# Kernel optimization log

Measured on AMD Instinct MI355X. Metric: run time of the kernel, lower is better.

## Reference

```python
import jax, jax.numpy as jnp
import numpy as np
import math

D_MODEL = 1024
N_HEAD = 16
D_FF = 4096
N_LAYERS = 4
SEQ = 2048
BATCH = 1
LN_EPS = 1e-5


def _pos_encoding(S, D, dtype):
    pos = jnp.arange(S, dtype=dtype)[:, None]                      # [S,1]
    div = jnp.exp(jnp.arange(0, D, 2, dtype=dtype) * (-math.log(10000.0) / D))
    ang = pos * div                                                 # [S,D/2]
    pe = jnp.stack([jnp.sin(ang), jnp.cos(ang)], axis=-1).reshape(S, D)  # interleave sin/cos
    return pe[:, None, :]                                           # [S,1,D]


def _layernorm(x, g, b):
    mu = jnp.mean(x, axis=-1, keepdims=True)
    var = jnp.mean(jnp.square(x - mu), axis=-1, keepdims=True)
    return (x - mu) * jax.lax.rsqrt(var + LN_EPS) * g + b


def setup_inputs() -> dict:
    key = jax.random.key(0)
    ks = jax.random.split(key, 16)
    f32 = jnp.float32
    L, D, F = N_LAYERS, D_MODEL, D_FF
    s = 0.02
    inp = {
        "X": jax.random.normal(ks[0], (SEQ, BATCH, D), dtype=f32),
        "Wqkv": jax.random.normal(ks[1], (L, 3 * D, D), dtype=f32) * s,
        "bqkv": jnp.zeros((L, 3 * D), dtype=f32),
        "Wo": jax.random.normal(ks[2], (L, D, D), dtype=f32) * s,
        "bo": jnp.zeros((L, D), dtype=f32),
        "ln1_g": jnp.ones((L, D), dtype=f32),
        "ln1_b": jnp.zeros((L, D), dtype=f32),
        "W1": jax.random.normal(ks[3], (L, F, D), dtype=f32) * s,
        "b1": jnp.zeros((L, F), dtype=f32),
        "W2": jax.random.normal(ks[4], (L, D, F), dtype=f32) * s,
        "b2": jnp.zeros((L, D), dtype=f32),
        "ln2_g": jnp.ones((L, D), dtype=f32),
        "ln2_b": jnp.zeros((L, D), dtype=f32),
        "Wdec": jax.random.normal(ks[5], (3, D), dtype=f32) * s,
        "bdec": jnp.zeros((3,), dtype=f32),
        "window_size": 128,
        "nhead": 16,
    }
    return inp


def reference(X, Wqkv, bqkv, Wo, bo, ln1_g, ln1_b, W1, b1, W2, b2, ln2_g, ln2_b, Wdec, bdec, window_size, nhead):
    S, B, D = X.shape
    H = nhead
    hd = D // H
    scale = 1.0 / math.sqrt(hd)

    x = X + _pos_encoding(S, D, X.dtype)  # dropout is identity at eval

    # banded additive mask: allowed iff |i-j| < window_size (triu/tril(-inf) construction)
    idx = jnp.arange(S)
    band = jnp.abs(idx[:, None] - idx[None, :]) < window_size
    mask = jnp.where(band, jnp.array(0.0, X.dtype), jnp.array(-jnp.inf, X.dtype))  # [S,S]

    L = Wqkv.shape[0]
    for l in range(L):
        # self-attention (post-norm encoder layer)
        qkv = jnp.einsum('sbd,ed->sbe', x, Wqkv[l]) + bqkv[l]
        q, k, v = jnp.split(qkv, 3, axis=-1)
        q = q.reshape(S, B, H, hd)
        k = k.reshape(S, B, H, hd)
        v = v.reshape(S, B, H, hd)
        scores = jnp.einsum('sbhd,tbhd->bhst', q, k) * scale + mask  # [B,H,S,S]
        attn = jax.nn.softmax(scores, axis=-1)
        o = jnp.einsum('bhst,tbhd->sbhd', attn, v).reshape(S, B, D)
        o = jnp.einsum('sbd,ed->sbe', o, Wo[l]) + bo[l]
        x = _layernorm(x + o, ln1_g[l], ln1_b[l])
        # feed-forward (relu)
        h = jax.nn.relu(jnp.einsum('sbd,fd->sbf', x, W1[l]) + b1[l])
        ff = jnp.einsum('sbf,df->sbd', h, W2[l]) + b2[l]
        x = _layernorm(x + ff, ln2_g[l], ln2_b[l])

    logits = jnp.einsum('sbd,cd->sbc', x, Wdec) + bdec  # [S,B,3]
    return jax.nn.log_softmax(logits, axis=-1)
```

## Files before the change

kernel.cpp:

```cpp
#include <hip/hip_runtime.h>
#include <hip/hip_bf16.h>
#include <cmath>

typedef __hip_bfloat16 bf16;
typedef __bf16 bf16x8 __attribute__((ext_vector_type(8)));
typedef __bf16 bf16x4 __attribute__((ext_vector_type(4)));
typedef float f32x4 __attribute__((ext_vector_type(4)));

typedef __attribute__((address_space(1))) void void_g;
typedef __attribute__((address_space(3))) void void_l;

#define SEQ 2048
#define DMODEL 1024
#define NHEAD 16
#define HDIM 64
#define DFF 4096
#define WINDOW 128
#define LN_EPS 1e-5f

__device__ __forceinline__ void gl_lds16(const bf16* g, bf16* l) {
    __builtin_amdgcn_global_load_lds((void_g*)(g), (void_l*)(l), 16, 0, 0);
}

__device__ __forceinline__ bf16x8 cvt8(float4 a, float4 b) {
    bf16x8 w;
    w[0] = (__bf16)a.x; w[1] = (__bf16)a.y; w[2] = (__bf16)a.z; w[3] = (__bf16)a.w;
    w[4] = (__bf16)b.x; w[5] = (__bf16)b.y; w[6] = (__bf16)b.z; w[7] = (__bf16)b.w;
    return w;
}

__global__ __launch_bounds__(256)
void add_pe(const float* __restrict__ X, bf16* __restrict__ x) {
    int idx = blockIdx.x * 256 + threadIdx.x;
    int s = idx >> 10, d = idx & 1023;
    float i2 = (float)(d & ~1);
    float div = expf(i2 * (-9.210340371976184f / 1024.0f));
    float ang = (float)s * div;
    float pe = (d & 1) ? cosf(ang) : sinf(ang);
    x[idx] = (bf16)(X[idx] + pe);
}

__global__ __launch_bounds__(256)
void cvt_w_layer(const float* __restrict__ wqkv, const float* __restrict__ wo,
                 const float* __restrict__ w1, const float* __restrict__ w2,
                 bf16* __restrict__ dst)
{
    int i = blockIdx.x * 256 + threadIdx.x;
    const float* src; size_t so;
    if (i < 393216)       { src = wqkv; so = (size_t)i * 8; }
    else if (i < 524288)  { src = wo;   so = (size_t)(i - 393216) * 8; }
    else if (i < 1048576) { src = w1;   so = (size_t)(i - 524288) * 8; }
    else                  { src = w2;   so = (size_t)(i - 1048576) * 8; }
    float4 a = *(const float4*)(src + so);
    float4 b = *(const float4*)(src + so + 4);
    *(bf16x8*)(dst + (size_t)i * 8) = cvt8(a, b);
}


#define G_PROLOGUE(Adecl, Wdecl)                                                 \
    __shared__ __align__(16) bf16 AS[2][128 * 64];                               \
    __shared__ __align__(16) bf16 BS[2][128 * 64];                               \
    const int tid  = threadIdx.x;                                                \
    const int lane = tid & 63;                                                   \
    const int wave = tid >> 6;                                                   \
    const int wm = wave >> 1, wn = wave & 1;                                     \
    const int r = lane & 15, quad = lane >> 4;                                   \
    const int rc = (quad ^ (r & 3)) * 8;                                         \
    f32x4 acc[4][4];                                                             \
    _Pragma("unroll")                                                            \
    for (int i = 0; i < 4; ++i)                                                  \
        _Pragma("unroll")                                                        \
        for (int j = 0; j < 4; ++j) acc[i][j] = (f32x4){0.f, 0.f, 0.f, 0.f};     \
    const bf16* Ap[4]; const bf16* Bp[4];                                        \
    _Pragma("unroll")                                                            \
    for (int i = 0; i < 4; ++i) {                                                \
        int c = tid + 256 * i;                                                   \
        int ks = c >> 9, row = (c >> 2) & 127, kch = (c & 3) ^ (row & 3);        \
        Ap[i] = (Adecl) + (size_t)(m0 + row) * K + ks * 32 + kch * 8;            \
        Bp[i] = (Wdecl) + (size_t)(n0 + row) * K + ks * 32 + kch * 8;            \
    }

#define G_STAGE(koff, Ad, Bd)                                                    \
    _Pragma("unroll")                                                            \
    for (int i = 0; i < 4; ++i)                                                  \
        gl_lds16(Ap[i] + (koff), (Ad) + (size_t)(tid + 256 * i) * 8);            \
    _Pragma("unroll")                                                            \
    for (int i = 0; i < 4; ++i)                                                  \
        gl_lds16(Bp[i] + (koff), (Bd) + (size_t)(tid + 256 * i) * 8);

#define G_KLOOP(Klim)                                                            \
    const int nit = (Klim) / 64;                                                 \
    bf16 *A_c = &AS[0][0], *A_n = &AS[1][0];                                     \
    bf16 *B_c = &BS[0][0], *B_n = &BS[1][0];                                     \
    G_STAGE(0, A_c, B_c)                                                         \
    asm volatile("s_waitcnt vmcnt(0)" ::: "memory");                             \
    __builtin_amdgcn_s_barrier();                                                \
    for (int t = 0; t < nit; ++t) {                                              \
        if (t + 1 < nit) { G_STAGE((t + 1) * 64, A_n, B_n) }                     \
        bf16x8 av[4][2], bv[4][2];                                               \
        _Pragma("unroll")                                                        \
        for (int mf = 0; mf < 4; ++mf)                                           \
            _Pragma("unroll")                                                    \
            for (int kk = 0; kk < 2; ++kk)                                       \
                av[mf][kk] = *(const bf16x8*)(A_c + kk * 4096 +                  \
                              (wm * 64 + mf * 16 + r) * 32 + rc);                \
        _Pragma("unroll")                                                        \
        for (int nf = 0; nf < 4; ++nf)                                           \
            _Pragma("unroll")                                                    \
            for (int kk = 0; kk < 2; ++kk)                                       \
                bv[nf][kk] = *(const bf16x8*)(B_c + kk * 4096 +                  \
                              (wn * 64 + nf * 16 + r) * 32 + rc);                \
        __builtin_amdgcn_s_setprio(1);                                           \
        _Pragma("unroll")                                                        \
        for (int mf = 0; mf < 4; ++mf)                                           \
            _Pragma("unroll")                                                    \
            for (int nf = 0; nf < 4; ++nf)                                       \
                _Pragma("unroll")                                                \
                for (int kk = 0; kk < 2; ++kk)                                   \
                    acc[mf][nf] = __builtin_amdgcn_mfma_f32_16x16x32_bf16(       \
                        av[mf][kk], bv[nf][kk], acc[mf][nf], 0, 0, 0);           \
        __builtin_amdgcn_s_setprio(0);                                           \
        asm volatile("s_waitcnt vmcnt(0)" ::: "memory");                         \
        __builtin_amdgcn_s_barrier();                                            \
        bf16* tA = A_c; A_c = A_n; A_n = tA;                                     \
        bf16* tB = B_c; B_c = B_n; B_n = tB;                                     \
    }

template<int ACT, int SX, int SY, int VOUT>
__global__ __launch_bounds__(256)
void gemm8_bt(const bf16* __restrict__ A, const bf16* __restrict__ W,
              const float* __restrict__ bias, bf16* __restrict__ C,
              bf16* __restrict__ Vt, int M, int N, int K)
{
    const int gx = gridDim.x;
    const int l = blockIdx.y * gx + blockIdx.x;
    const int k = l & 7, j = l >> 3;
    const int xg = gx / SX;
    const int tx = (k % xg) * SX + (j % SX);
    const int ty = (k / xg) * SY + (j / SX);
    const int m0 = ty * 128, n0 = tx * 128;
    G_PROLOGUE(A, W)
    G_KLOOP(K)
    if (VOUT && n0 >= 2048) {
#pragma unroll
        for (int nt = 0; nt < 4; ++nt) {
            int n = n0 + wn * 64 + nt * 16 + r;
            float bv = bias[n];
            int dv = n - 2048;
#pragma unroll
            for (int mt = 0; mt < 4; ++mt) {
                int m = m0 + wm * 64 + mt * 16 + quad * 4;
                bf16x4 pk;
#pragma unroll
                for (int e = 0; e < 4; ++e) pk[e] = (__bf16)(acc[mt][nt][e] + bv);
                *(bf16x4*)(Vt + (size_t)dv * SEQ + m) = pk;
            }
        }
    } else {
#pragma unroll
        for (int nt = 0; nt < 4; ++nt) {
            int n = n0 + wn * 64 + nt * 16 + r;
            float bv = bias[n];
#pragma unroll
            for (int mt = 0; mt < 4; ++mt) {
#pragma unroll
                for (int e = 0; e < 4; ++e) {
                    int m = m0 + wm * 64 + mt * 16 + quad * 4 + e;
                    float v = acc[mt][nt][e] + bv;
                    if (ACT == 1) v = fmaxf(v, 0.f);
                    C[(size_t)m * N + n] = (bf16)v;
                }
            }
        }
    }
}

template<int SPLIT, int SY>
__global__ __launch_bounds__(256)
void gemm8_splitk(const bf16* __restrict__ A, const bf16* __restrict__ Wfull,
                  float* __restrict__ Cacc, int M, int N, int K)
{
    const int gx = gridDim.x, gy = gridDim.y;
    const int l = (blockIdx.z * gy + blockIdx.y) * gx + blockIdx.x;
    const int k = l & 7, j = l >> 3;
    const int yg = gy / SY;
    const int tx = j % gx;
    const int ty = (k % yg) * SY + (j / gx);
    const int tz = k / yg;
    const int m0 = ty * 128, n0 = tx * 128;
    const int Kc = K / SPLIT;
    const bf16* Ab = A + (size_t)tz * Kc;
    const bf16* W = Wfull + (size_t)tz * Kc;
    float* Cz = Cacc + (size_t)tz * M * N;
    G_PROLOGUE(Ab, W)
    G_KLOOP(Kc)
#pragma unroll
    for (int nt = 0; nt < 4; ++nt) {
        int n = n0 + wn * 64 + nt * 16 + r;
#pragma unroll
        for (int mt = 0; mt < 4; ++mt) {
#pragma unroll
            for (int e = 0; e < 4; ++e) {
                int m = m0 + wm * 64 + mt * 16 + quad * 4 + e;
                Cz[(size_t)m * N + n] = acc[mt][nt][e];
            }
        }
    }
}

__global__ __launch_bounds__(256)
void attn_mfma(const bf16* __restrict__ qkv, const bf16* __restrict__ Vt,
               bf16* __restrict__ o)
{
    __shared__ __align__(16) __bf16 Plds[4][16 * 40];
    const int tid = threadIdx.x, lane = tid & 63, w = tid >> 6;
    const int h = blockIdx.x & 15;
    const int qw = (blockIdx.x >> 4) * 64 + w * 16;
    const int r = lane & 15, quad = lane >> 4;
    __bf16* P = Plds[w];

    bf16x8 qa[2];
    {
        const bf16* qrow = qkv + (size_t)(qw + r) * 3072 + h * 64 + quad * 8;
#pragma unroll
        for (int c = 0; c < 2; ++c) {
            bf16x8 t = *(const bf16x8*)(qrow + c * 32);
#pragma unroll
            for (int j = 0; j < 8; ++j) qa[c][j] = (__bf16)((float)t[j] * 0.125f);
        }
    }

    bf16x8 ones;
#pragma unroll
    for (int j = 0; j < 8; ++j) ones[j] = (__bf16)1.0f;

    f32x4 acc[4];
#pragma unroll
    for (int d = 0; d < 4; ++d) acc[d] = (f32x4){0.f, 0.f, 0.f, 0.f};
    float m_run[4], l_run[4];
#pragma unroll
    for (int e = 0; e < 4; ++e) { m_run[e] = -1e30f; l_run[e] = 0.f; }

    int jmin = qw - (WINDOW - 1); if (jmin < 0) jmin = 0;
    int jmax = qw + 15 + (WINDOW - 1); if (jmax > SEQ - 1) jmax = SEQ - 1;

    for (int kt = jmin & ~31; kt <= jmax; kt += 32) {
        f32x4 S[2];
#pragma unroll
        for (int c = 0; c < 2; ++c) {
            const bf16* krow = qkv + (size_t)(kt + 16 * c + r) * 3072 + 1024 + h * 64 + quad * 8;
            bf16x8 kb0 = *(const bf16x8*)(krow);
            bf16x8 kb1 = *(const bf16x8*)(krow + 32);
            f32x4 s = (f32x4){0.f, 0.f, 0.f, 0.f};
            s = __builtin_amdgcn_mfma_f32_16x16x32_bf16(qa[0], kb0, s, 0, 0, 0);
            s = __builtin_amdgcn_mfma_f32_16x16x32_bf16(qa[1], kb1, s, 0, 0, 0);
            S[c] = s;
        }
#pragma unroll
        for (int c = 0; c < 2; ++c)
#pragma unroll
            for (int e = 0; e < 4; ++e) {
                int j = kt + 16 * c + r;
                int i = qw + quad * 4 + e;
                bool valid = (unsigned)(j - i + (WINDOW - 1)) <= (unsigned)(2 * WINDOW - 2);
                S[c][e] = valid ? S[c][e] : -1e30f;
            }
        float alpha[4], mnew[4];
#pragma unroll
        for (int e = 0; e < 4; ++e) {
            float v = fmaxf(S[0][e], S[1][e]);
#pragma unroll
            for (int off = 1; off <= 8; off <<= 1) v = fmaxf(v, __shfl_xor(v, off, 64));
            mnew[e] = fmaxf(m_run[e], v);
            alpha[e] = __expf(m_run[e] - mnew[e]);
            m_run[e] = mnew[e];
        }
#pragma unroll
        for (int c = 0; c < 2; ++c)
#pragma unroll
            for (int e = 0; e < 4; ++e) {
                float p = __expf(S[c][e] - mnew[e]);
                p = (S[c][e] <= -1e29f) ? 0.f : p;
                P[(quad * 4 + e) * 40 + 16 * c + r] = (__bf16)p;
            }
        bf16x8 pa = *(const bf16x8*)(P + r * 40 + quad * 8);
#pragma unroll
        for (int d = 0; d < 4; ++d)
#pragma unroll
            for (int e = 0; e < 4; ++e) acc[d][e] *= alpha[e];
        f32x4 ls = (f32x4){0.f, 0.f, 0.f, 0.f};
        ls = __builtin_amdgcn_mfma_f32_16x16x32_bf16(pa, ones, ls, 0, 0, 0);
#pragma unroll
        for (int e = 0; e < 4; ++e) l_run[e] = l_run[e] * alpha[e] + ls[e];
#pragma unroll
        for (int d = 0; d < 4; ++d) {
            const bf16* vrow = Vt + (size_t)(h * 64 + 16 * d + r) * SEQ + kt + quad * 8;
            bf16x8 vb = *(const bf16x8*)(vrow);
            acc[d] = __builtin_amdgcn_mfma_f32_16x16x32_bf16(pa, vb, acc[d], 0, 0, 0);
        }
    }

#pragma unroll
    for (int d = 0; d < 4; ++d)
#pragma unroll
        for (int e = 0; e < 4; ++e) {
            int i = qw + quad * 4 + e;
            o[(size_t)i * DMODEL + h * 64 + 16 * d + r] = (bf16)(acc[d][e] / l_run[e]);
        }
}

__global__ __launch_bounds__(256)
void ln_residual_f32(bf16* __restrict__ x, const float* __restrict__ accd,
                     const float* __restrict__ bias,
                     const float* __restrict__ gamma, const float* __restrict__ beta)
{
    const int s = blockIdx.x, tid = threadIdx.x;
    const int lane = tid & 63, wave = tid >> 6;
    __shared__ float red[8];
    float v[4];
    float sum = 0.f;
#pragma unroll
    for (int i = 0; i < 4; ++i) {
        int d = i * 256 + tid;
        float a = accd[(size_t)s * 1024 + d]
                + accd[(size_t)SEQ * 1024 + (size_t)s * 1024 + d]
                + accd[2 * (size_t)SEQ * 1024 + (size_t)s * 1024 + d]
                + accd[3 * (size_t)SEQ * 1024 + (size_t)s * 1024 + d];
        v[i] = (float)x[(size_t)s * 1024 + d] + a + bias[d];
        sum += v[i];
    }
#pragma unroll
    for (int off = 32; off; off >>= 1) sum += __shfl_xor(sum, off, 64);
    if (lane == 0) red[wave] = sum;
    __syncthreads();
    float mu = (red[0] + red[1] + red[2] + red[3]) * (1.f / 1024.f);
    float sq = 0.f;
#pragma unroll
    for (int i = 0; i < 4; ++i) { float t = v[i] - mu; sq += t * t; }
#pragma unroll
    for (int off = 32; off; off >>= 1) sq += __shfl_xor(sq, off, 64);
    if (lane == 0) red[wave + 4] = sq;
    __syncthreads();
    float var = (red[4] + red[5] + red[6] + red[7]) * (1.f / 1024.f);
    float inv = rsqrtf(var + LN_EPS);
#pragma unroll
    for (int i = 0; i < 4; ++i) {
        int d = i * 256 + tid;
        x[(size_t)s * 1024 + d] = (bf16)((v[i] - mu) * inv * gamma[d] + beta[d]);
    }
}

__global__ __launch_bounds__(256)
void decoder(const bf16* __restrict__ x, const float* __restrict__ Wdec,
             const float* __restrict__ bdec, float* __restrict__ out)
{
    const int s = blockIdx.x * 4 + (threadIdx.x >> 6);
    const int lane = threadIdx.x & 63;
    float a0 = 0.f, a1 = 0.f, a2 = 0.f;
    for (int d = lane; d < 1024; d += 64) {
        float xv = (float)x[(size_t)s * 1024 + d];
        a0 += xv * Wdec[d];
        a1 += xv * Wdec[1024 + d];
        a2 += xv * Wdec[2048 + d];
    }
#pragma unroll
    for (int off = 32; off; off >>= 1) {
        a0 += __shfl_xor(a0, off, 64);
        a1 += __shfl_xor(a1, off, 64);
        a2 += __shfl_xor(a2, off, 64);
    }
    if (lane == 0) {
        float z0 = a0 + bdec[0];
        float z1 = a1 + bdec[1];
        float z2 = a2 + bdec[2];
        float mx = fmaxf(z0, fmaxf(z1, z2));
        float lse = mx + logf(__expf(z0 - mx) + __expf(z1 - mx) + __expf(z2 - mx));
        out[s * 3 + 0] = z0 - lse;
        out[s * 3 + 1] = z1 - lse;
        out[s * 3 + 2] = z2 - lse;
    }
}

extern "C" void kernel_launch(void* const* d_in, const int* in_sizes, int n_in,
                              void* d_out, int out_size, void* d_ws, size_t ws_size,
                              hipStream_t stream)
{
    const float* X    = (const float*)d_in[0];
    const float* Wqkv = (const float*)d_in[1];
    const float* bqkv = (const float*)d_in[2];
    const float* Wo   = (const float*)d_in[3];
    const float* bo   = (const float*)d_in[4];
    const float* ln1g = (const float*)d_in[5];
    const float* ln1b = (const float*)d_in[6];
    const float* W1   = (const float*)d_in[7];
    const float* b1   = (const float*)d_in[8];
    const float* W2   = (const float*)d_in[9];
    const float* b2   = (const float*)d_in[10];
    const float* ln2g = (const float*)d_in[11];
    const float* ln2b = (const float*)d_in[12];
    const float* Wdec = (const float*)d_in[13];
    const float* bdec = (const float*)d_in[14];

    bf16* ws   = (bf16*)d_ws;
    bf16* x    = ws;
    bf16* buf  = x   + (size_t)SEQ * DMODEL;
    bf16* qkv  = buf;
    bf16* ao   = buf + (size_t)SEQ * 3 * DMODEL;
    bf16* h    = buf;
    bf16* Vt   = buf + (size_t)SEQ * DFF;
    float* accf = (float*)(Vt + (size_t)SEQ * DMODEL);
    bf16* Wb   = (bf16*)(accf + 4 * (size_t)SEQ * DMODEL);
    bf16* WoB  = Wb + 3145728;
    bf16* W1B  = Wb + 4194304;
    bf16* W2B  = Wb + 8388608;

    add_pe<<<(SEQ * DMODEL) / 256, 256, 0, stream>>>(X, x);

    for (int l = 0; l < 4; ++l) {
        cvt_w_layer<<<6144, 256, 0, stream>>>(
            Wqkv + (size_t)l * 3145728, Wo + (size_t)l * 1048576,
            W1 + (size_t)l * 4194304,  W2 + (size_t)l * 4194304, Wb);
        gemm8_bt<0, 6, 8, 1><<<dim3(3072 / 128, SEQ / 128), 256, 0, stream>>>(
            x, Wb, bqkv + l * 3072, qkv, Vt, SEQ, 3072, 1024);
        attn_mfma<<<(SEQ / 64) * NHEAD, 256, 0, stream>>>(qkv, Vt, ao);
        gemm8_splitk<4, 8><<<dim3(1024 / 128, SEQ / 128, 4), 256, 0, stream>>>(
            ao, WoB, accf, SEQ, 1024, 1024);
        ln_residual_f32<<<SEQ, 256, 0, stream>>>(x, accf, bo + l * 1024,
                                                 ln1g + l * 1024, ln1b + l * 1024);
        gemm8_bt<1, 8, 8, 0><<<dim3(4096 / 128, SEQ / 128), 256, 0, stream>>>(
            x, W1B, b1 + l * 4096, h, nullptr, SEQ, 4096, 1024);
        gemm8_splitk<4, 8><<<dim3(1024 / 128, SEQ / 128, 4), 256, 0, stream>>>(
            h, W2B, accf, SEQ, 1024, 4096);
        ln_residual_f32<<<SEQ, 256, 0, stream>>>(x, accf, b2 + l * 1024,
                                                 ln2g + l * 1024, ln2b + l * 1024);
    }

    decoder<<<SEQ / 4, 256, 0, stream>>>(x, Wdec, bdec, (float*)d_out);
}
```

Measured before the change: 730.9 us.

## Retune GEMM tiling: 64-row QKV tiles, 8-way single-buffered FF2 split-K

The QKV projection now uses 64x128 tiles, doubling the grid to 768 blocks for better CU coverage. The FF2 GEMM moves from 4-way to 8-way split-K with a single-buffered LDS kernel, which adds blocks and cuts LDS per block for occupancy but loses load/compute overlap. The split-K accumulator workspace doubles and the LayerNorm kernel now sums 8 partials, adding memory traffic in exchange for more parallelism.

```diff
diff --git a/kernel.cpp b/kernel.cpp
--- a/kernel.cpp
+++ b/kernel.cpp
@@ -56,8 +56,7 @@
     *(bf16x8*)(dst + (size_t)i * 8) = cvt8(a, b);
 }
 
-
-#define G_PROLOGUE(Adecl, Wdecl)                                                 \
+#define GA_PROLOGUE(Adecl, Wdecl)                                                \
     __shared__ __align__(16) bf16 AS[2][128 * 64];                               \
     __shared__ __align__(16) bf16 BS[2][128 * 64];                               \
     const int tid  = threadIdx.x;                                                \
@@ -80,7 +79,7 @@
         Bp[i] = (Wdecl) + (size_t)(n0 + row) * K + ks * 32 + kch * 8;            \
     }
 
-#define G_STAGE(koff, Ad, Bd)                                                    \
+#define GA_STAGE(koff, Ad, Bd)                                                   \
     _Pragma("unroll")                                                            \
     for (int i = 0; i < 4; ++i)                                                  \
         gl_lds16(Ap[i] + (koff), (Ad) + (size_t)(tid + 256 * i) * 8);            \
@@ -88,22 +87,137 @@
     for (int i = 0; i < 4; ++i)                                                  \
         gl_lds16(Bp[i] + (koff), (Bd) + (size_t)(tid + 256 * i) * 8);
 
-#define G_KLOOP(Klim)                                                            \
+#define GA_COMPUTE(Ab_, Bb_)                                                     \
+    bf16x8 av[4][2], bv[4][2];                                                   \
+    _Pragma("unroll")                                                            \
+    for (int mf = 0; mf < 4; ++mf)                                               \
+        _Pragma("unroll")                                                        \
+        for (int kk = 0; kk < 2; ++kk)                                           \
+            av[mf][kk] = *(const bf16x8*)((Ab_) + kk * 4096 +                    \
+                          (wm * 64 + mf * 16 + r) * 32 + rc);                    \
+    _Pragma("unroll")                                                            \
+    for (int nf = 0; nf < 4; ++nf)                                               \
+        _Pragma("unroll")                                                        \
+        for (int kk = 0; kk < 2; ++kk)                                           \
+            bv[nf][kk] = *(const bf16x8*)((Bb_) + kk * 4096 +                    \
+                          (wn * 64 + nf * 16 + r) * 32 + rc);                    \
+    __builtin_amdgcn_s_setprio(1);                                               \
+    _Pragma("unroll")                                                            \
+    for (int mf = 0; mf < 4; ++mf)                                               \
+        _Pragma("unroll")                                                        \
+        for (int nf = 0; nf < 4; ++nf)                                           \
+            _Pragma("unroll")                                                    \
+            for (int kk = 0; kk < 2; ++kk)                                       \
+                acc[mf][nf] = __builtin_amdgcn_mfma_f32_16x16x32_bf16(           \
+                    av[mf][kk], bv[nf][kk], acc[mf][nf], 0, 0, 0);               \
+    __builtin_amdgcn_s_setprio(0);
+
+#define GA_KLOOP(Klim)                                                           \
     const int nit = (Klim) / 64;                                                 \
     bf16 *A_c = &AS[0][0], *A_n = &AS[1][0];                                     \
     bf16 *B_c = &BS[0][0], *B_n = &BS[1][0];                                     \
-    G_STAGE(0, A_c, B_c)                                                         \
+    GA_STAGE(0, A_c, B_c)                                                        \
     asm volatile("s_waitcnt vmcnt(0)" ::: "memory");                             \
     __builtin_amdgcn_s_barrier();                                                \
     for (int t = 0; t < nit; ++t) {                                              \
-        if (t + 1 < nit) { G_STAGE((t + 1) * 64, A_n, B_n) }                     \
-        bf16x8 av[4][2], bv[4][2];                                               \
-        _Pragma("unroll")                                                        \
-        for (int mf = 0; mf < 4; ++mf)                                           \
+        if (t + 1 < nit) { GA_STAGE((t + 1) * 64, A_n, B_n) }                    \
+        { GA_COMPUTE(A_c, B_c) }                                                 \
+        asm volatile("s_waitcnt vmcnt(0)" ::: "memory");                         \
+        __builtin_amdgcn_s_barrier();                                            \
+        bf16* tA = A_c; A_c = A_n; A_n = tA;                                     \
+        bf16* tB = B_c; B_c = B_n; B_n = tB;                                     \
+    }
+
+#define GC_PROLOGUE(Adecl, Wdecl)                                                \
+    __shared__ __align__(16) bf16 AS1[128 * 64];                                 \
+    __shared__ __align__(16) bf16 BS1[128 * 64];                                 \
+    const int tid  = threadIdx.x;                                                \
+    const int lane = tid & 63;                                                   \
+    const int wave = tid >> 6;                                                   \
+    const int wm = wave >> 1, wn = wave & 1;                                     \
+    const int r = lane & 15, quad = lane >> 4;                                   \
+    const int rc = (quad ^ (r & 3)) * 8;                                         \
+    f32x4 acc[4][4];                                                             \
+    _Pragma("unroll")                                                            \
+    for (int i = 0; i < 4; ++i)                                                  \
+        _Pragma("unroll")                                                        \
+        for (int j = 0; j < 4; ++j) acc[i][j] = (f32x4){0.f, 0.f, 0.f, 0.f};     \
+    const bf16* Ap[4]; const bf16* Bp[4];                                        \
+    _Pragma("unroll")                                                            \
+    for (int i = 0; i < 4; ++i) {                                                \
+        int c = tid + 256 * i;                                                   \
+        int ks = c >> 9, row = (c >> 2) & 127, kch = (c & 3) ^ (row & 3);        \
+        Ap[i] = (Adecl) + (size_t)(m0 + row) * K + ks * 32 + kch * 8;            \
+        Bp[i] = (Wdecl) + (size_t)(n0 + row) * K + ks * 32 + kch * 8;            \
+    }
+
+#define GC_KLOOP(Klim)                                                           \
+    const int nit = (Klim) / 64;                                                 \
+    for (int t = 0; t < nit; ++t) {                                              \
+        _Pragma("unroll")                                                        \
+        for (int i = 0; i < 4; ++i)                                              \
+            gl_lds16(Ap[i] + t * 64, AS1 + (size_t)(tid + 256 * i) * 8);         \
+        _Pragma("unroll")                                                        \
+        for (int i = 0; i < 4; ++i)                                              \
+            gl_lds16(Bp[i] + t * 64, BS1 + (size_t)(tid + 256 * i) * 8);         \
+        asm volatile("s_waitcnt vmcnt(0)" ::: "memory");                         \
+        __builtin_amdgcn_s_barrier();                                            \
+        { GA_COMPUTE(AS1, BS1) }                                                 \
+        __builtin_amdgcn_s_barrier();                                            \
+    }
+
+#define GB_PROLOGUE(Adecl, Wdecl)                                                \
+    __shared__ __align__(16) bf16 AS[2][64 * 64];                                \
+    __shared__ __align__(16) bf16 BS[2][128 * 64];                               \
+    const int tid  = threadIdx.x;                                                \
+    const int lane = tid & 63;                                                   \
+    const int wave = tid >> 6;                                                   \
+    const int wm = wave >> 1, wn = wave & 1;                                     \
+    const int r = lane & 15, quad = lane >> 4;                                   \
+    const int rc = (quad ^ (r & 3)) * 8;                                         \
+    f32x4 acc[2][4];                                                             \
+    _Pragma("unroll")                                                            \
+    for (int i = 0; i < 2; ++i)                                                  \
+        _Pragma("unroll")                                                        \
+        for (int j = 0; j < 4; ++j) acc[i][j] = (f32x4){0.f, 0.f, 0.f, 0.f};     \
+    const bf16* Ap[2]; const bf16* Bp[4];                                        \
+    _Pragma("unroll")                                                            \
+    for (int i = 0; i < 2; ++i) {                                                \
+        int c = tid + 256 * i;                                                   \
+        int ks = c >> 8, row = (c >> 2) & 63, kch = (c & 3) ^ (row & 3);         \
+        Ap[i] = (Adecl) + (size_t)(m0 + row) * K + ks * 32 + kch * 8;            \
+    }                                                                            \
+    _Pragma("unroll")                                                            \
+    for (int i = 0; i < 4; ++i) {                                                \
+        int c = tid + 256 * i;                                                   \
+        int ks = c >> 9, row = (c >> 2) & 127, kch = (c & 3) ^ (row & 3);        \
+        Bp[i] = (Wdecl) + (size_t)(n0 + row) * K + ks * 32 + kch * 8;            \
+    }
+
+#define GB_STAGE(koff, Ad, Bd)                                                   \
+    _Pragma("unroll")                                                            \
+    for (int i = 0; i < 2; ++i)                                                  \
+        gl_lds16(Ap[i] + (koff), (Ad) + (size_t)(tid + 256 * i) * 8);            \
+    _Pragma("unroll")                                                            \
+    for (int i = 0; i < 4; ++i)                                                  \
+        gl_lds16(Bp[i] + (koff), (Bd) + (size_t)(tid + 256 * i) * 8);
+
+#define GB_KLOOP(Klim)                                                           \
+    const int nit = (Klim) / 64;                                                 \
+    bf16 *A_c = &AS[0][0], *A_n = &AS[1][0];                                     \
+    bf16 *B_c = &BS[0][0], *B_n = &BS[1][0];                                     \
+    GB_STAGE(0, A_c, B_c)                                                        \
+    asm volatile("s_waitcnt vmcnt(0)" ::: "memory");                             \
+    __builtin_amdgcn_s_barrier();                                                \
+    for (int t = 0; t < nit; ++t) {                                              \
+        if (t + 1 < nit) { GB_STAGE((t + 1) * 64, A_n, B_n) }                    \
+        bf16x8 av[2][2], bv[4][2];                                               \
+        _Pragma("unroll")                                                        \
+        for (int mf = 0; mf < 2; ++mf)                                           \
             _Pragma("unroll")                                                    \
             for (int kk = 0; kk < 2; ++kk)                                       \
-                av[mf][kk] = *(const bf16x8*)(A_c + kk * 4096 +                  \
-                              (wm * 64 + mf * 16 + r) * 32 + rc);                \
+                av[mf][kk] = *(const bf16x8*)(A_c + kk * 2048 +                  \
+                              (wm * 32 + mf * 16 + r) * 32 + rc);                \
         _Pragma("unroll")                                                        \
         for (int nf = 0; nf < 4; ++nf)                                           \
             _Pragma("unroll")                                                    \
@@ -112,7 +226,7 @@
                               (wn * 64 + nf * 16 + r) * 32 + rc);                \
         __builtin_amdgcn_s_setprio(1);                                           \
         _Pragma("unroll")                                                        \
-        for (int mf = 0; mf < 4; ++mf)                                           \
+        for (int mf = 0; mf < 2; ++mf)                                           \
             _Pragma("unroll")                                                    \
             for (int nf = 0; nf < 4; ++nf)                                       \
                 _Pragma("unroll")                                                \
@@ -126,11 +240,58 @@
         bf16* tB = B_c; B_c = B_n; B_n = tB;                                     \
     }
 
-template<int ACT, int SX, int SY, int VOUT>
-__global__ __launch_bounds__(256)
-void gemm8_bt(const bf16* __restrict__ A, const bf16* __restrict__ W,
+template<int SX, int SY>
+__global__ __launch_bounds__(256)
+void gemm_qkv(const bf16* __restrict__ A, const bf16* __restrict__ W,
               const float* __restrict__ bias, bf16* __restrict__ C,
               bf16* __restrict__ Vt, int M, int N, int K)
+{
+    const int gx = gridDim.x;
+    const int l = blockIdx.y * gx + blockIdx.x;
+    const int k = l & 7, j = l >> 3;
+    const int xg = gx / SX;
+    const int tx = (k % xg) * SX + (j % SX);
+    const int ty = (k / xg) * SY + (j / SX);
+    const int m0 = ty * 64, n0 = tx * 128;
+    GB_PROLOGUE(A, W)
+    GB_KLOOP(K)
+    if (n0 >= 2048) {
+#pragma unroll
+        for (int nt = 0; nt < 4; ++nt) {
+            int n = n0 + wn * 64 + nt * 16 + r;
+            float bv = bias[n];
+            int dv = n - 2048;
+#pragma unroll
+            for (int mt = 0; mt < 2; ++mt) {
+                int m = m0 + wm * 32 + mt * 16 + quad * 4;
+                bf16x4 pk;
+#pragma unroll
+                for (int e = 0; e < 4; ++e) pk[e] = (__bf16)(acc[mt][nt][e] + bv);
+                *(bf16x4*)(Vt + (size_t)dv * SEQ + m) = pk;
+            }
+        }
+    } else {
+#pragma unroll
+        for (int nt = 0; nt < 4; ++nt) {
+            int n = n0 + wn * 64 + nt * 16 + r;
+            float bv = bias[n];
+#pragma unroll
+            for (int mt = 0; mt < 2; ++mt) {
+#pragma unroll
+                for (int e = 0; e < 4; ++e) {
+                    int m = m0 + wm * 32 + mt * 16 + quad * 4 + e;
+                    C[(size_t)m * N + n] = (bf16)(acc[mt][nt][e] + bv);
+                }
+            }
+        }
+    }
+}
+
+template<int SX, int SY>
+__global__ __launch_bounds__(256)
+void gemm_ff1(const bf16* __restrict__ A, const bf16* __restrict__ W,
+              const float* __restrict__ bias, bf16* __restrict__ C,
+              int M, int N, int K)
 {
     const int gx = gridDim.x;
     const int l = blockIdx.y * gx + blockIdx.x;
@@ -139,46 +300,27 @@
     const int tx = (k % xg) * SX + (j % SX);
     const int ty = (k / xg) * SY + (j / SX);
     const int m0 = ty * 128, n0 = tx * 128;
-    G_PROLOGUE(A, W)
-    G_KLOOP(K)
-    if (VOUT && n0 >= 2048) {
-#pragma unroll
-        for (int nt = 0; nt < 4; ++nt) {
-            int n = n0 + wn * 64 + nt * 16 + r;
-            float bv = bias[n];
-            int dv = n - 2048;
-#pragma unroll
-            for (int mt = 0; mt < 4; ++mt) {
-                int m = m0 + wm * 64 + mt * 16 + quad * 4;
-                bf16x4 pk;
-#pragma unroll
-                for (int e = 0; e < 4; ++e) pk[e] = (__bf16)(acc[mt][nt][e] + bv);
-                *(bf16x4*)(Vt + (size_t)dv * SEQ + m) = pk;
+    GA_PROLOGUE(A, W)
+    GA_KLOOP(K)
+#pragma unroll
+    for (int nt = 0; nt < 4; ++nt) {
+        int n = n0 + wn * 64 + nt * 16 + r;
+        float bv = bias[n];
+#pragma unroll
+        for (int mt = 0; mt < 4; ++mt) {
+#pragma unroll
+            for (int e = 0; e < 4; ++e) {
+                int m = m0 + wm * 64 + mt * 16 + quad * 4 + e;
+                C[(size_t)m * N + n] = (bf16)fmaxf(acc[mt][nt][e] + bv, 0.f);
             }
         }
-    } else {
-#pragma unroll
-        for (int nt = 0; nt < 4; ++nt) {
-            int n = n0 + wn * 64 + nt * 16 + r;
-            float bv = bias[n];
-#pragma unroll
-            for (int mt = 0; mt < 4; ++mt) {
-#pragma unroll
-                for (int e = 0; e < 4; ++e) {
-                    int m = m0 + wm * 64 + mt * 16 + quad * 4 + e;
-                    float v = acc[mt][nt][e] + bv;
-                    if (ACT == 1) v = fmaxf(v, 0.f);
-                    C[(size_t)m * N + n] = (bf16)v;
-                }
-            }
-        }
     }
 }
 
 template<int SPLIT, int SY>
 __global__ __launch_bounds__(256)
-void gemm8_splitk(const bf16* __restrict__ A, const bf16* __restrict__ Wfull,
-                  float* __restrict__ Cacc, int M, int N, int K)
+void gemm_splitk_db(const bf16* __restrict__ A, const bf16* __restrict__ Wfull,
+                    float* __restrict__ Cacc, int M, int N, int K)
 {
     const int gx = gridDim.x, gy = gridDim.y;
     const int l = (blockIdx.z * gy + blockIdx.y) * gx + blockIdx.x;
@@ -192,8 +334,41 @@
     const bf16* Ab = A + (size_t)tz * Kc;
     const bf16* W = Wfull + (size_t)tz * Kc;
     float* Cz = Cacc + (size_t)tz * M * N;
-    G_PROLOGUE(Ab, W)
-    G_KLOOP(Kc)
+    GA_PROLOGUE(Ab, W)
+    GA_KLOOP(Kc)
+#pragma unroll
+    for (int nt = 0; nt < 4; ++nt) {
+        int n = n0 + wn * 64 + nt * 16 + r;
+#pragma unroll
+        for (int mt = 0; mt < 4; ++mt) {
+#pragma unroll
+            for (int e = 0; e < 4; ++e) {
+                int m = m0 + wm * 64 + mt * 16 + quad * 4 + e;
+                Cz[(size_t)m * N + n] = acc[mt][nt][e];
+            }
+        }
+    }
+}
+
+template<int SPLIT, int SY>
+__global__ __launch_bounds__(256)
+void gemm_splitk_sb(const bf16* __restrict__ A, const bf16* __restrict__ Wfull,
+                    float* __restrict__ Cacc, int M, int N, int K)
+{
+    const int gx = gridDim.x, gy = gridDim.y;
+    const int l = (blockIdx.z * gy + blockIdx.y) * gx + blockIdx.x;
+    const int k = l & 7, j = l >> 3;
+    const int yg = gy / SY;
+    const int tx = j % gx;
+    const int ty = (k % yg) * SY + (j / gx);
+    const int tz = k / yg;
+    const int m0 = ty * 128, n0 = tx * 128;
+    const int Kc = K / SPLIT;
+    const bf16* Ab = A + (size_t)tz * Kc;
+    const bf16* W = Wfull + (size_t)tz * Kc;
+    float* Cz = Cacc + (size_t)tz * M * N;
+    GC_PROLOGUE(Ab, W)
+    GC_KLOOP(Kc)
 #pragma unroll
     for (int nt = 0; nt < 4; ++nt) {
         int n = n0 + wn * 64 + nt * 16 + r;
@@ -309,6 +484,7 @@
         }
 }
 
+template<int NP>
 __global__ __launch_bounds__(256)
 void ln_residual_f32(bf16* __restrict__ x, const float* __restrict__ accd,
                      const float* __restrict__ bias,
@@ -322,10 +498,10 @@
 #pragma unroll
     for (int i = 0; i < 4; ++i) {
         int d = i * 256 + tid;
-        float a = accd[(size_t)s * 1024 + d]
-                + accd[(size_t)SEQ * 1024 + (size_t)s * 1024 + d]
-                + accd[2 * (size_t)SEQ * 1024 + (size_t)s * 1024 + d]
-                + accd[3 * (size_t)SEQ * 1024 + (size_t)s * 1024 + d];
+        float a = 0.f;
+#pragma unroll
+        for (int p = 0; p < NP; ++p)
+            a += accd[(size_t)p * SEQ * 1024 + (size_t)s * 1024 + d];
         v[i] = (float)x[(size_t)s * 1024 + d] + a + bias[d];
         sum += v[i];
     }
@@ -409,7 +585,7 @@
     bf16* h    = buf;
     bf16* Vt   = buf + (size_t)SEQ * DFF;
     float* accf = (float*)(Vt + (size_t)SEQ * DMODEL);
-    bf16* Wb   = (bf16*)(accf + 4 * (size_t)SEQ * DMODEL);
+    bf16* Wb   = (bf16*)(accf + 8 * (size_t)SEQ * DMODEL);
     bf16* WoB  = Wb + 3145728;
     bf16* W1B  = Wb + 4194304;
     bf16* W2B  = Wb + 8388608;
@@ -420,19 +596,19 @@
         cvt_w_layer<<<6144, 256, 0, stream>>>(
             Wqkv + (size_t)l * 3145728, Wo + (size_t)l * 1048576,
             W1 + (size_t)l * 4194304,  W2 + (size_t)l * 4194304, Wb);
-        gemm8_bt<0, 6, 8, 1><<<dim3(3072 / 128, SEQ / 128), 256, 0, stream>>>(
+        gemm_qkv<6, 16><<<dim3(3072 / 128, SEQ / 64), 256, 0, stream>>>(
             x, Wb, bqkv + l * 3072, qkv, Vt, SEQ, 3072, 1024);
         attn_mfma<<<(SEQ / 64) * NHEAD, 256, 0, stream>>>(qkv, Vt, ao);
-        gemm8_splitk<4, 8><<<dim3(1024 / 128, SEQ / 128, 4), 256, 0, stream>>>(
+        gemm_splitk_db<4, 8><<<dim3(1024 / 128, SEQ / 128, 4), 256, 0, stream>>>(
             ao, WoB, accf, SEQ, 1024, 1024);
-        ln_residual_f32<<<SEQ, 256, 0, stream>>>(x, accf, bo + l * 1024,
-                                                 ln1g + l * 1024, ln1b + l * 1024);
-        gemm8_bt<1, 8, 8, 0><<<dim3(4096 / 128, SEQ / 128), 256, 0, stream>>>(
-            x, W1B, b1 + l * 4096, h, nullptr, SEQ, 4096, 1024);
-        gemm8_splitk<4, 8><<<dim3(1024 / 128, SEQ / 128, 4), 256, 0, stream>>>(
+        ln_residual_f32<4><<<SEQ, 256, 0, stream>>>(x, accf, bo + l * 1024,
+                                                    ln1g + l * 1024, ln1b + l * 1024);
+        gemm_ff1<8, 8><<<dim3(4096 / 128, SEQ / 128), 256, 0, stream>>>(
+            x, W1B, b1 + l * 4096, h, SEQ, 4096, 1024);
+        gemm_splitk_sb<8, 16><<<dim3(1024 / 128, SEQ / 128, 8), 256, 0, stream>>>(
             h, W2B, accf, SEQ, 1024, 4096);
-        ln_residual_f32<<<SEQ, 256, 0, stream>>>(x, accf, b2 + l * 1024,
-                                                 ln2g + l * 1024, ln2b + l * 1024);
+        ln_residual_f32<8><<<SEQ, 256, 0, stream>>>(x, accf, b2 + l * 1024,
+                                                    ln2g + l * 1024, ln2b + l * 1024);
     }
 
     decoder<<<SEQ / 4, 256, 0, stream>>>(x, Wdec, bdec, (float*)d_out);
```

Measured after the change: 762.8 us. 4.4% more time.
